# Performance work log

Measured on AMD Instinct MI355X. Metric: run time of the kernel, lower is better.

## Reference

```python
import jax, jax.numpy as jnp
import numpy as np

D_MODEL = 512
B, T = 2, 4096
LN_EPS = 1e-5


def _layernorm(x, gamma, beta):
    mu = jnp.mean(x, axis=-1, keepdims=True)
    var = jnp.mean((x - mu) ** 2, axis=-1, keepdims=True)
    return (x - mu) * jax.lax.rsqrt(var + LN_EPS) * gamma + beta


def setup_inputs() -> dict:
    key = jax.random.key(0)
    ks = jax.random.split(key, 16)
    d = D_MODEL
    s = 1.0 / np.sqrt(d)
    inp = {
        "tokens": jax.random.normal(ks[0], (B, T, d), dtype=jnp.float32),
        "Wq": jax.random.normal(ks[1], (d, d), dtype=jnp.float32) * s,
        "bq": jnp.zeros((d,), jnp.float32),
        "Wk": jax.random.normal(ks[2], (d, d), dtype=jnp.float32) * s,
        "bk": jnp.zeros((d,), jnp.float32),
        "Wv": jax.random.normal(ks[3], (d, d), dtype=jnp.float32) * s,
        "bv": jnp.zeros((d,), jnp.float32),
        "distance_scale": jnp.asarray(0.01, jnp.float32),
        "W1": jax.random.normal(ks[4], (d, 4 * d), dtype=jnp.float32) * s,
        "b1": jnp.zeros((4 * d,), jnp.float32),
        "W2": jax.random.normal(ks[5], (4 * d, d), dtype=jnp.float32) * (1.0 / np.sqrt(4 * d)),
        "b2": jnp.zeros((d,), jnp.float32),
        "g1": jnp.ones((d,), jnp.float32),
        "be1": jnp.zeros((d,), jnp.float32),
        "g2": jnp.ones((d,), jnp.float32),
        "be2": jnp.zeros((d,), jnp.float32),
    }
    return inp


def reference(tokens, Wq, bq, Wk, bk, Wv, bv, distance_scale,
              W1, b1, W2, b2, g1, be1, g2, be2):
    Bv, Tv, d = tokens.shape
    q = tokens @ Wq + bq
    k = tokens @ Wk + bk
    v = tokens @ Wv + bv
    # [B, T, T] raw scores
    scores = jnp.einsum('btd,bsd->bts', q, k)
    pos = jnp.arange(Tv)
    distance = jnp.abs(pos[None, :] - pos[:, None]).astype(jnp.float32)  # [T, T]
    scores = scores + (-distance_scale * distance)[None, :, :]
    causal = pos[None, :] > pos[:, None]  # strict upper triangle
    scores = jnp.where(causal[None, :, :], -jnp.inf, scores)
    scores = scores / jnp.sqrt(jnp.asarray(d, jnp.float32))
    attn = jax.nn.softmax(scores, axis=-1)
    attn_out = jnp.einsum('bts,bsd->btd', attn, v)
    x = _layernorm(tokens + attn_out, g1, be1)
    y = jnp.maximum(x @ W1 + b1, 0.0) @ W2 + b2
    z = _layernorm(y + x, g2, be2)
    return z
```

## Files before the change

### kernel.cpp

```cpp
#include <hip/hip_runtime.h>
#include <hip/hip_bf16.h>
#include <math.h>

typedef unsigned short u16;
typedef __attribute__((ext_vector_type(8))) short short8;
typedef __attribute__((ext_vector_type(4))) float float4v;

#define MFMA_BF16(a, b, c) __builtin_amdgcn_mfma_f32_16x16x32_bf16((a), (b), (c), 0, 0, 0)

typedef const __attribute__((address_space(1))) void* gas_ptr;
typedef __attribute__((address_space(3))) void* las_ptr;

__device__ __forceinline__ u16 f2bf(float f) {
  __hip_bfloat16 h = __float2bfloat16(f);
  return __builtin_bit_cast(u16, h);
}

__device__ __forceinline__ float bf2f(u16 v) {
  return __builtin_bit_cast(float, (unsigned)v << 16);
}

__device__ __forceinline__ void load_lds16(const u16* g, u16* l) {
  __builtin_amdgcn_global_load_lds((gas_ptr)g, (las_ptr)l, 16, 0, 0);
}

__device__ __forceinline__ int xcd_swz(int bid, int nwg) {
  return (bid & 7) * (nwg >> 3) + (bid >> 3);
}

__device__ __forceinline__ void gemm_mainloop(
    const u16* __restrict__ A, const u16* __restrict__ Bt,
    int kb, int kend, int lda, int ldb,
    int m0, int n0, u16* As, u16* Bs, float4v acc[4][4])
{
  const int tid = threadIdx.x;
  const int w = tid >> 6, lane = tid & 63;
  const int wr = w >> 1, wc = w & 1;
  const int lr = lane & 15, lk = (lane >> 4) * 8;
  for (int k0 = kb; k0 < kend; k0 += 32) {
#pragma unroll
    for (int c = 0; c < 2; ++c) {
      int idx = c * 256 + w * 64 + lane;
      int r = idx >> 2, c8 = idx & 3;
      load_lds16(A + (size_t)(m0 + r) * lda + k0 + c8 * 8, As + (size_t)(c * 256 + w * 64) * 8);
      load_lds16(Bt + (size_t)(n0 + r) * ldb + k0 + c8 * 8, Bs + (size_t)(c * 256 + w * 64) * 8);
    }
    __syncthreads();
    short8 af[4], bf[4];
#pragma unroll
    for (int mt = 0; mt < 4; ++mt)
      af[mt] = *(const short8*)&As[(wr * 64 + mt * 16 + lr) * 32 + lk];
#pragma unroll
    for (int nt = 0; nt < 4; ++nt)
      bf[nt] = *(const short8*)&Bs[(wc * 64 + nt * 16 + lr) * 32 + lk];
#pragma unroll
    for (int mt = 0; mt < 4; ++mt)
#pragma unroll
      for (int nt = 0; nt < 4; ++nt)
        acc[mt][nt] = MFMA_BF16(af[mt], bf[nt], acc[mt][nt]);
    __syncthreads();
  }
}

__global__ __launch_bounds__(256) void gemm_qkv(
    const u16* __restrict__ A, const u16* __restrict__ Bt,
    const float* __restrict__ bq, const float* __restrict__ bk, const float* __restrict__ bv,
    u16* __restrict__ qo, u16* __restrict__ ko, u16* __restrict__ vto)
{
  __shared__ u16 As[128 * 32], Bs[128 * 32];
  float4v acc[4][4];
#pragma unroll
  for (int mt = 0; mt < 4; ++mt)
#pragma unroll
    for (int nt = 0; nt < 4; ++nt) acc[mt][nt] = (float4v){0.f, 0.f, 0.f, 0.f};
  const int s = xcd_swz(blockIdx.x + 12 * blockIdx.y, 12 * 64);
  const int m0 = (s / 12) * 128, n0 = (s % 12) * 128;
  gemm_mainloop(A, Bt, 0, 512, 512, 512, m0, n0, As, Bs, acc);
  const int tid = threadIdx.x, w = tid >> 6, lane = tid & 63;
  const int wr = w >> 1, wc = w & 1, lr = lane & 15, lg = lane >> 4;
#pragma unroll
  for (int mt = 0; mt < 4; ++mt) {
#pragma unroll
    for (int nt = 0; nt < 4; ++nt) {
      int n = n0 + wc * 64 + nt * 16 + lr;
#pragma unroll
      for (int r = 0; r < 4; ++r) {
        int i = m0 + wr * 64 + mt * 16 + lg * 4 + r;
        float v = acc[mt][nt][r];
        if (n < 512) {
          qo[(size_t)i * 512 + n] = f2bf(v + bq[n]);
        } else if (n < 1024) {
          ko[(size_t)i * 512 + (n - 512)] = f2bf(v + bk[n - 512]);
        } else {
          int bb = i >> 12, t = i & 4095;
          vto[((size_t)(bb * 512 + (n - 1024))) * 4096 + t] = f2bf(v + bv[n - 1024]);
        }
      }
    }
  }
}

__global__ __launch_bounds__(256) void gemm_qk_p(
    const u16* __restrict__ q, const u16* __restrict__ k,
    const float* __restrict__ dsp,
    u16* __restrict__ P, float* __restrict__ l)
{
  __shared__ u16 As[128 * 32], Bs[128 * 32];
  float4v acc[4][4];
#pragma unroll
  for (int mt = 0; mt < 4; ++mt)
#pragma unroll
    for (int nt = 0; nt < 4; ++nt) acc[mt][nt] = (float4v){0.f, 0.f, 0.f, 0.f};
  const int b = blockIdx.y;
  const u16* qb = q + (size_t)b * 4096 * 512;
  const u16* kb = k + (size_t)b * 4096 * 512;
  u16* Pb = P + (size_t)b * 4096 * 4096;
  float* lb = l + b * 4096;
  int idx = blockIdx.x;
  int tm = (int)((sqrtf(8.0f * (float)idx + 1.0f) - 1.0f) * 0.5f);
  while ((tm + 1) * (tm + 2) / 2 <= idx) ++tm;
  while (tm * (tm + 1) / 2 > idx) --tm;
  int tn = idx - tm * (tm + 1) / 2;
  const int m0 = tm * 128, n0 = tn * 128;
  gemm_mainloop(qb, kb, 0, 512, 512, 512, m0, n0, As, Bs, acc);
  const int tid = threadIdx.x, w = tid >> 6, lane = tid & 63;
  const int wr = w >> 1, wc = w & 1, lr = lane & 15, lg = lane >> 4;
  const float invs = 0.04419417382415922f;
  const float dsi = dsp[0] * invs;
  const float L2E = 1.4426950408889634f;
  float rs[4][4];
#pragma unroll
  for (int mt = 0; mt < 4; ++mt)
#pragma unroll
    for (int r = 0; r < 4; ++r) rs[mt][r] = 0.f;
#pragma unroll
  for (int mt = 0; mt < 4; ++mt) {
#pragma unroll
    for (int nt = 0; nt < 4; ++nt) {
      int j = n0 + wc * 64 + nt * 16 + lr;
#pragma unroll
      for (int r = 0; r < 4; ++r) {
        int i = m0 + wr * 64 + mt * 16 + lg * 4 + r;
        float x = acc[mt][nt][r] * invs - dsi * fabsf((float)(i - j));
        float p = (j > i) ? 0.f : exp2f(x * L2E);
        Pb[(size_t)i * 4096 + j] = f2bf(p);
        rs[mt][r] += p;
      }
    }
  }
#pragma unroll
  for (int mt = 0; mt < 4; ++mt) {
#pragma unroll
    for (int r = 0; r < 4; ++r) {
      float v = rs[mt][r];
#pragma unroll
      for (int off = 1; off < 16; off <<= 1) v += __shfl_xor(v, off, 64);
      if (lr == 0)
        atomicAdd(&lb[m0 + wr * 64 + mt * 16 + lg * 4 + r], v);
    }
  }
}

__global__ __launch_bounds__(256) void gemm_pv(
    const u16* __restrict__ P, const u16* __restrict__ vt,
    float* __restrict__ y0, u16* __restrict__ y1,
    u16* __restrict__ y2, u16* __restrict__ y3)
{
  __shared__ u16 As[128 * 32], Bs[128 * 32];
  float4v acc[4][4];
#pragma unroll
  for (int mt = 0; mt < 4; ++mt)
#pragma unroll
    for (int nt = 0; nt < 4; ++nt) acc[mt][nt] = (float4v){0.f, 0.f, 0.f, 0.f};
  const int s = xcd_swz(blockIdx.x + 4 * (blockIdx.y + 80 * blockIdx.z), 640);
  const int b = s / 320;
  const int t2 = s % 320;
  const int xb = t2 % 4;
  int rem = t2 / 4;
  const u16* Pb = P + (size_t)b * 4096 * 4096;
  const u16* vb = vt + (size_t)b * 512 * 4096;
  int tm = 0, cpt = 1;
  while (rem >= cpt) { rem -= cpt; ++tm; cpt = (tm >> 3) + 1; }
  const int m0 = tm * 128, n0 = xb * 128;
  const int kb = rem * 1024;
  const int kfull = (tm + 1) * 128;
  const int kend = (kb + 1024 < kfull) ? (kb + 1024) : kfull;
  gemm_mainloop(Pb, vb, kb, kend, 4096, 4096, m0, n0, As, Bs, acc);
  const int tid = threadIdx.x, w = tid >> 6, lane = tid & 63;
  const int wr = w >> 1, wc = w & 1, lr = lane & 15, lg = lane >> 4;
  const size_t bofs = (size_t)b * 4096 * 512;
#pragma unroll
  for (int mt = 0; mt < 4; ++mt) {
#pragma unroll
    for (int nt = 0; nt < 4; ++nt) {
      int n = n0 + wc * 64 + nt * 16 + lr;
#pragma unroll
      for (int r = 0; r < 4; ++r) {
        int i = m0 + wr * 64 + mt * 16 + lg * 4 + r;
        size_t o = bofs + (size_t)i * 512 + n;
        float v = acc[mt][nt][r];
        if (rem == 0)      y0[o] = v;
        else if (rem == 1) y1[o] = f2bf(v);
        else if (rem == 2) y2[o] = f2bf(v);
        else               y3[o] = f2bf(v);
      }
    }
  }
}

__global__ __launch_bounds__(256) void gemm_ffn1(
    const u16* __restrict__ A, const u16* __restrict__ Bt,
    const float* __restrict__ b1, u16* __restrict__ h)
{
  __shared__ u16 As[128 * 32], Bs[128 * 32];
  float4v acc[4][4];
#pragma unroll
  for (int mt = 0; mt < 4; ++mt)
#pragma unroll
    for (int nt = 0; nt < 4; ++nt) acc[mt][nt] = (float4v){0.f, 0.f, 0.f, 0.f};
  const int s = xcd_swz(blockIdx.x + 16 * blockIdx.y, 16 * 64);
  const int m0 = (s / 16) * 128, n0 = (s % 16) * 128;
  gemm_mainloop(A, Bt, 0, 512, 512, 512, m0, n0, As, Bs, acc);
  const int tid = threadIdx.x, w = tid >> 6, lane = tid & 63;
  const int wr = w >> 1, wc = w & 1, lr = lane & 15, lg = lane >> 4;
#pragma unroll
  for (int mt = 0; mt < 4; ++mt) {
#pragma unroll
    for (int nt = 0; nt < 4; ++nt) {
      int n = n0 + wc * 64 + nt * 16 + lr;
#pragma unroll
      for (int r = 0; r < 4; ++r) {
        int i = m0 + wr * 64 + mt * 16 + lg * 4 + r;
        h[(size_t)i * 2048 + n] = f2bf(fmaxf(acc[mt][nt][r] + b1[n], 0.f));
      }
    }
  }
}

__global__ __launch_bounds__(256) void gemm_ffn2(
    const u16* __restrict__ A, const u16* __restrict__ Bt,
    float* __restrict__ f0, u16* __restrict__ f1)
{
  __shared__ u16 As[128 * 32], Bs[128 * 32];
  float4v acc[4][4];
#pragma unroll
  for (int mt = 0; mt < 4; ++mt)
#pragma unroll
    for (int nt = 0; nt < 4; ++nt) acc[mt][nt] = (float4v){0.f, 0.f, 0.f, 0.f};
  const int s = xcd_swz(blockIdx.x + 4 * (blockIdx.y + 64 * blockIdx.z), 512);
  const int zz = s / 256;
  const int t2 = s % 256;
  const int m0 = (t2 / 4) * 128, n0 = (t2 % 4) * 128;
  const int kb = zz * 1024;
  gemm_mainloop(A, Bt, kb, kb + 1024, 2048, 2048, m0, n0, As, Bs, acc);
  const int tid = threadIdx.x, w = tid >> 6, lane = tid & 63;
  const int wr = w >> 1, wc = w & 1, lr = lane & 15, lg = lane >> 4;
#pragma unroll
  for (int mt = 0; mt < 4; ++mt) {
#pragma unroll
    for (int nt = 0; nt < 4; ++nt) {
      int n = n0 + wc * 64 + nt * 16 + lr;
#pragma unroll
      for (int r = 0; r < 4; ++r) {
        int i = m0 + wr * 64 + mt * 16 + lg * 4 + r;
        if (zz == 0) f0[(size_t)i * 512 + n] = acc[mt][nt][r];
        else         f1[(size_t)i * 512 + n] = f2bf(acc[mt][nt][r]);
      }
    }
  }
}

__global__ __launch_bounds__(256) void ln1_kernel(
    const float* __restrict__ y0, const u16* __restrict__ y1,
    const u16* __restrict__ y2, const u16* __restrict__ y3,
    const float* __restrict__ lsum, const float* __restrict__ tok,
    const float* __restrict__ g, const float* __restrict__ be,
    float* __restrict__ of, u16* __restrict__ ob)
{
  const int row = blockIdx.x * 4 + (threadIdx.x >> 6);
  const int lane = threadIdx.x & 63;
  const int rloc = row & 4095;
  const size_t base = (size_t)row * 512 + lane * 8;
  const float linv = 1.0f / lsum[row];
  float v[8];
#pragma unroll
  for (int t = 0; t < 8; ++t) v[t] = y0[base + t];
  if (rloc >= 1024) {
#pragma unroll
    for (int t = 0; t < 8; ++t) v[t] += bf2f(y1[base + t]);
  }
  if (rloc >= 2048) {
#pragma unroll
    for (int t = 0; t < 8; ++t) v[t] += bf2f(y2[base + t]);
  }
  if (rloc >= 3072) {
#pragma unroll
    for (int t = 0; t < 8; ++t) v[t] += bf2f(y3[base + t]);
  }
#pragma unroll
  for (int t = 0; t < 8; ++t) v[t] = v[t] * linv + tok[base + t];
  float s = 0.f;
#pragma unroll
  for (int t = 0; t < 8; ++t) s += v[t];
#pragma unroll
  for (int off = 1; off < 64; off <<= 1) s += __shfl_xor(s, off, 64);
  const float mu = s * (1.0f / 512.0f);
  float qv = 0.f;
#pragma unroll
  for (int t = 0; t < 8; ++t) { float d = v[t] - mu; qv += d * d; }
#pragma unroll
  for (int off = 1; off < 64; off <<= 1) qv += __shfl_xor(qv, off, 64);
  const float rs = rsqrtf(qv * (1.0f / 512.0f) + 1e-5f);
  const int cb = lane * 8;
#pragma unroll
  for (int t = 0; t < 8; ++t) {
    float xv = (v[t] - mu) * rs * g[cb + t] + be[cb + t];
    of[base + t] = xv;
    ob[base + t] = f2bf(xv);
  }
}

__global__ __launch_bounds__(256) void ln2_kernel(
    const float* __restrict__ f0, const u16* __restrict__ f1,
    const float* __restrict__ b2, const float* __restrict__ bsrc,
    const float* __restrict__ g, const float* __restrict__ be,
    float* __restrict__ of)
{
  const int row = blockIdx.x * 4 + (threadIdx.x >> 6);
  const int lane = threadIdx.x & 63;
  const size_t base = (size_t)row * 512 + lane * 8;
  const int cb = lane * 8;
  float v[8];
#pragma unroll
  for (int t = 0; t < 8; ++t)
    v[t] = f0[base + t] + bf2f(f1[base + t]) + b2[cb + t] + bsrc[base + t];
  float s = 0.f;
#pragma unroll
  for (int t = 0; t < 8; ++t) s += v[t];
#pragma unroll
  for (int off = 1; off < 64; off <<= 1) s += __shfl_xor(s, off, 64);
  const float mu = s * (1.0f / 512.0f);
  float qv = 0.f;
#pragma unroll
  for (int t = 0; t < 8; ++t) { float d = v[t] - mu; qv += d * d; }
#pragma unroll
  for (int off = 1; off < 64; off <<= 1) qv += __shfl_xor(qv, off, 64);
  const float rs = rsqrtf(qv * (1.0f / 512.0f) + 1e-5f);
#pragma unroll
  for (int t = 0; t < 8; ++t) {
    float xv = (v[t] - mu) * rs * g[cb + t] + be[cb + t];
    of[base + t] = xv;
  }
}

__global__ __launch_bounds__(256) void cast_bf_kernel(
    const float* __restrict__ in, u16* __restrict__ out)
{
  const size_t i = ((size_t)blockIdx.x * 256 + threadIdx.x) * 8;
#pragma unroll
  for (int t = 0; t < 8; ++t) out[i + t] = f2bf(in[i + t]);
}

__global__ __launch_bounds__(256) void transpose_qkv_kernel(
    const float* __restrict__ Wq, const float* __restrict__ Wk,
    const float* __restrict__ Wv, u16* __restrict__ dst)
{
  __shared__ u16 tile[32][33];
  const float* src = (blockIdx.z == 0) ? Wq : (blockIdx.z == 1) ? Wk : Wv;
  u16* d = dst + (size_t)blockIdx.z * 512 * 512;
  const int tx = threadIdx.x & 31, ty = threadIdx.x >> 5;
  const int n0 = blockIdx.x * 32, k0 = blockIdx.y * 32;
#pragma unroll
  for (int i = 0; i < 32; i += 8)
    tile[ty + i][tx] = f2bf(src[(size_t)(k0 + ty + i) * 512 + n0 + tx]);
  __syncthreads();
#pragma unroll
  for (int i = 0; i < 32; i += 8)
    d[(size_t)(n0 + ty + i) * 512 + k0 + tx] = tile[tx][ty + i];
}

__global__ __launch_bounds__(256) void transpose_bf_kernel(
    const float* __restrict__ src, u16* __restrict__ dst, int K, int N)
{
  __shared__ u16 tile[32][33];
  const int tx = threadIdx.x & 31, ty = threadIdx.x >> 5;
  const int n0 = blockIdx.x * 32, k0 = blockIdx.y * 32;
#pragma unroll
  for (int i = 0; i < 32; i += 8)
    tile[ty + i][tx] = f2bf(src[(size_t)(k0 + ty + i) * N + n0 + tx]);
  __syncthreads();
#pragma unroll
  for (int i = 0; i < 32; i += 8)
    dst[(size_t)(n0 + ty + i) * K + k0 + tx] = tile[tx][ty + i];
}

extern "C" void kernel_launch(void* const* d_in, const int* in_sizes, int n_in,
                              void* d_out, int out_size, void* d_ws, size_t ws_size,
                              hipStream_t stream) {
  const float* tokens = (const float*)d_in[0];
  const float* Wq = (const float*)d_in[1];
  const float* bq = (const float*)d_in[2];
  const float* Wk = (const float*)d_in[3];
  const float* bk = (const float*)d_in[4];
  const float* Wv = (const float*)d_in[5];
  const float* bv = (const float*)d_in[6];
  const float* dscale = (const float*)d_in[7];
  const float* W1 = (const float*)d_in[8];
  const float* b1 = (const float*)d_in[9];
  const float* W2 = (const float*)d_in[10];
  const float* b2 = (const float*)d_in[11];
  const float* g1 = (const float*)d_in[12];
  const float* be1 = (const float*)d_in[13];
  const float* g2 = (const float*)d_in[14];
  const float* be2 = (const float*)d_in[15];
  float* out = (float*)d_out;

  char* ws = (char*)d_ws;
  u16*   tok_bf = (u16*)(ws + 0);
  u16*   wqkvT  = (u16*)(ws + 8388608);
  u16*   w1T    = (u16*)(ws + 9961472);
  u16*   w2T    = (u16*)(ws + 12058624);
  u16*   qbuf   = (u16*)(ws + 14155776);
  u16*   kbuf   = (u16*)(ws + 22544384);
  u16*   vtbuf  = (u16*)(ws + 30932992);
  u16*   Pbuf   = (u16*)(ws + 39321600);
  float* y0buf  = (float*)(ws + 106430464);
  u16*   y1buf  = (u16*)(ws + 123207680);
  u16*   y2buf  = (u16*)(ws + 131596288);
  u16*   y3buf  = (u16*)(ws + 139984896);
  float* xf     = (float*)(ws + 148373504);
  u16*   xbf    = (u16*)(ws + 165150720);
  u16*   hbuf   = (u16*)(ws + 173539328);
  float* f0buf  = (float*)(ws + 207093760);
  u16*   f1buf  = (u16*)(ws + 223870976);
  float* lbuf   = (float*)(ws + 232259584);

  (void)hipMemsetAsync(lbuf, 0, 2 * 4096 * sizeof(float), stream);

  cast_bf_kernel<<<2048, 256, 0, stream>>>(tokens, tok_bf);
  transpose_qkv_kernel<<<dim3(16, 16, 3), 256, 0, stream>>>(Wq, Wk, Wv, wqkvT);
  transpose_bf_kernel<<<dim3(64, 16), 256, 0, stream>>>(W1, w1T, 512, 2048);
  transpose_bf_kernel<<<dim3(16, 64), 256, 0, stream>>>(W2, w2T, 2048, 512);

  gemm_qkv<<<dim3(12, 64), 256, 0, stream>>>(tok_bf, wqkvT, bq, bk, bv, qbuf, kbuf, vtbuf);

  gemm_qk_p<<<dim3(528, 2), 256, 0, stream>>>(qbuf, kbuf, dscale, Pbuf, lbuf);
  gemm_pv<<<dim3(4, 80, 2), 256, 0, stream>>>(Pbuf, vtbuf, y0buf, y1buf, y2buf, y3buf);

  ln1_kernel<<<2048, 256, 0, stream>>>(y0buf, y1buf, y2buf, y3buf, lbuf, tokens,
                                       g1, be1, xf, xbf);

  gemm_ffn1<<<dim3(16, 64), 256, 0, stream>>>(xbf, w1T, b1, hbuf);

  gemm_ffn2<<<dim3(4, 64, 2), 256, 0, stream>>>(hbuf, w2T, f0buf, f1buf);

  ln2_kernel<<<2048, 256, 0, stream>>>(f0buf, f1buf, b2, xf, g2, be2, out);
}
```

Baseline: 305.6 us.

## Use 256x256 double-buffered GEMM tiles with 512 threads across all matmuls

Replaces the 128x128, BK=32 single-buffered mainloop with a 256x256, BK=64 tile computed by 8 waves. It double-buffers LDS through async global-to-LDS loads and raises MFMA priority with setprio. All GEMM kernels are relaunched with the new grid decompositions, and FFN2 now uses a 4-way split-K with extra partial buffers that ln2 sums. The larger tiles aim to raise arithmetic intensity and hide load latency. In exchange they use 128KB of dynamic LDS per block and 128 accumulator registers per thread, and launch far fewer blocks, which can hurt occupancy and load balance.

```diff
diff --git a/kernel.cpp b/kernel.cpp
--- a/kernel.cpp
+++ b/kernel.cpp
@@ -28,64 +28,86 @@
   return (bid & 7) * (nwg >> 3) + (bid >> 3);
 }
 
-__device__ __forceinline__ void gemm_mainloop(
+__device__ __forceinline__ void gemm_mainloop256(
     const u16* __restrict__ A, const u16* __restrict__ Bt,
     int kb, int kend, int lda, int ldb,
-    int m0, int n0, u16* As, u16* Bs, float4v acc[4][4])
+    int m0, int n0, u16* lds, float4v acc[8][4])
 {
   const int tid = threadIdx.x;
   const int w = tid >> 6, lane = tid & 63;
-  const int wr = w >> 1, wc = w & 1;
+  const int wr = w >> 2, wc = w & 3;
   const int lr = lane & 15, lk = (lane >> 4) * 8;
-  for (int k0 = kb; k0 < kend; k0 += 32) {
-#pragma unroll
-    for (int c = 0; c < 2; ++c) {
-      int idx = c * 256 + w * 64 + lane;
-      int r = idx >> 2, c8 = idx & 3;
-      load_lds16(A + (size_t)(m0 + r) * lda + k0 + c8 * 8, As + (size_t)(c * 256 + w * 64) * 8);
-      load_lds16(Bt + (size_t)(n0 + r) * ldb + k0 + c8 * 8, Bs + (size_t)(c * 256 + w * 64) * 8);
+  const int r4 = lane >> 2, c4 = (lane & 3) * 8;
+
+  auto stage = [&](int buf, int k0) {
+#pragma unroll
+    for (int c = 0; c < 4; ++c) {
+      int ri = w + c * 8;
+      int p = ri >> 4, rg = ri & 15;
+      int row = rg * 16 + r4;
+      int col = p * 32 + c4;
+      u16* dA = lds + buf * 16384 + p * 8192 + rg * 512;
+      u16* dB = lds + 32768 + buf * 16384 + p * 8192 + rg * 512;
+      load_lds16(A + (size_t)(m0 + row) * lda + k0 + col, dA);
+      load_lds16(Bt + (size_t)(n0 + row) * ldb + k0 + col, dB);
+    }
+  };
+
+  int cur = 0;
+  stage(0, kb);
+  __syncthreads();
+  for (int k0 = kb; k0 < kend; k0 += 64) {
+    if (k0 + 64 < kend) stage(cur ^ 1, k0 + 64);
+    const u16* As = lds + cur * 16384;
+    const u16* Bs = lds + 32768 + cur * 16384;
+#pragma unroll
+    for (int ks = 0; ks < 2; ++ks) {
+      short8 af[8], bfr[4];
+#pragma unroll
+      for (int mt = 0; mt < 8; ++mt)
+        af[mt] = *(const short8*)&As[ks * 8192 + (wr * 128 + mt * 16 + lr) * 32 + lk];
+#pragma unroll
+      for (int nt = 0; nt < 4; ++nt)
+        bfr[nt] = *(const short8*)&Bs[ks * 8192 + (wc * 64 + nt * 16 + lr) * 32 + lk];
+      __builtin_amdgcn_s_setprio(1);
+#pragma unroll
+      for (int mt = 0; mt < 8; ++mt)
+#pragma unroll
+        for (int nt = 0; nt < 4; ++nt)
+          acc[mt][nt] = MFMA_BF16(af[mt], bfr[nt], acc[mt][nt]);
+      __builtin_amdgcn_s_setprio(0);
     }
     __syncthreads();
-    short8 af[4], bf[4];
-#pragma unroll
-    for (int mt = 0; mt < 4; ++mt)
-      af[mt] = *(const short8*)&As[(wr * 64 + mt * 16 + lr) * 32 + lk];
-#pragma unroll
-    for (int nt = 0; nt < 4; ++nt)
-      bf[nt] = *(const short8*)&Bs[(wc * 64 + nt * 16 + lr) * 32 + lk];
-#pragma unroll
-    for (int mt = 0; mt < 4; ++mt)
-#pragma unroll
-      for (int nt = 0; nt < 4; ++nt)
-        acc[mt][nt] = MFMA_BF16(af[mt], bf[nt], acc[mt][nt]);
-    __syncthreads();
-  }
-}
-
-__global__ __launch_bounds__(256) void gemm_qkv(
+    cur ^= 1;
+  }
+}
+
+#define ACC_INIT(acc)                                              \
+  _Pragma("unroll") for (int mt = 0; mt < 8; ++mt)                 \
+  _Pragma("unroll") for (int nt = 0; nt < 4; ++nt)                 \
+      acc[mt][nt] = (float4v){0.f, 0.f, 0.f, 0.f};
+
+__global__ __launch_bounds__(512, 2) void gemm_qkv(
     const u16* __restrict__ A, const u16* __restrict__ Bt,
     const float* __restrict__ bq, const float* __restrict__ bk, const float* __restrict__ bv,
     u16* __restrict__ qo, u16* __restrict__ ko, u16* __restrict__ vto)
 {
-  __shared__ u16 As[128 * 32], Bs[128 * 32];
-  float4v acc[4][4];
-#pragma unroll
-  for (int mt = 0; mt < 4; ++mt)
-#pragma unroll
-    for (int nt = 0; nt < 4; ++nt) acc[mt][nt] = (float4v){0.f, 0.f, 0.f, 0.f};
-  const int s = xcd_swz(blockIdx.x + 12 * blockIdx.y, 12 * 64);
-  const int m0 = (s / 12) * 128, n0 = (s % 12) * 128;
-  gemm_mainloop(A, Bt, 0, 512, 512, 512, m0, n0, As, Bs, acc);
+  extern __shared__ u16 lds[];
+  float4v acc[8][4];
+  ACC_INIT(acc);
+  const int s = xcd_swz(blockIdx.x, 192);
+  const int m0 = (s / 6) * 256, n0 = (s % 6) * 256;
+  gemm_mainloop256(A, Bt, 0, 512, 512, 512, m0, n0, lds, acc);
   const int tid = threadIdx.x, w = tid >> 6, lane = tid & 63;
-  const int wr = w >> 1, wc = w & 1, lr = lane & 15, lg = lane >> 4;
-#pragma unroll
-  for (int mt = 0; mt < 4; ++mt) {
+  const int wr = w >> 2, wc = w & 3, lr = lane & 15, lg = lane >> 4;
+#pragma unroll
+  for (int mt = 0; mt < 8; ++mt) {
 #pragma unroll
     for (int nt = 0; nt < 4; ++nt) {
       int n = n0 + wc * 64 + nt * 16 + lr;
 #pragma unroll
       for (int r = 0; r < 4; ++r) {
-        int i = m0 + wr * 64 + mt * 16 + lg * 4 + r;
+        int i = m0 + wr * 128 + mt * 16 + lg * 4 + r;
         float v = acc[mt][nt][r];
         if (n < 512) {
           qo[(size_t)i * 512 + n] = f2bf(v + bq[n]);
@@ -100,17 +122,14 @@
   }
 }
 
-__global__ __launch_bounds__(256) void gemm_qk_p(
+__global__ __launch_bounds__(512, 2) void gemm_qk_p(
     const u16* __restrict__ q, const u16* __restrict__ k,
     const float* __restrict__ dsp,
     u16* __restrict__ P, float* __restrict__ l)
 {
-  __shared__ u16 As[128 * 32], Bs[128 * 32];
-  float4v acc[4][4];
-#pragma unroll
-  for (int mt = 0; mt < 4; ++mt)
-#pragma unroll
-    for (int nt = 0; nt < 4; ++nt) acc[mt][nt] = (float4v){0.f, 0.f, 0.f, 0.f};
+  extern __shared__ u16 lds[];
+  float4v acc[8][4];
+  ACC_INIT(acc);
   const int b = blockIdx.y;
   const u16* qb = q + (size_t)b * 4096 * 512;
   const u16* kb = k + (size_t)b * 4096 * 512;
@@ -121,26 +140,26 @@
   while ((tm + 1) * (tm + 2) / 2 <= idx) ++tm;
   while (tm * (tm + 1) / 2 > idx) --tm;
   int tn = idx - tm * (tm + 1) / 2;
-  const int m0 = tm * 128, n0 = tn * 128;
-  gemm_mainloop(qb, kb, 0, 512, 512, 512, m0, n0, As, Bs, acc);
+  const int m0 = tm * 256, n0 = tn * 256;
+  gemm_mainloop256(qb, kb, 0, 512, 512, 512, m0, n0, lds, acc);
   const int tid = threadIdx.x, w = tid >> 6, lane = tid & 63;
-  const int wr = w >> 1, wc = w & 1, lr = lane & 15, lg = lane >> 4;
+  const int wr = w >> 2, wc = w & 3, lr = lane & 15, lg = lane >> 4;
   const float invs = 0.04419417382415922f;
   const float dsi = dsp[0] * invs;
   const float L2E = 1.4426950408889634f;
-  float rs[4][4];
-#pragma unroll
-  for (int mt = 0; mt < 4; ++mt)
+  float rs[8][4];
+#pragma unroll
+  for (int mt = 0; mt < 8; ++mt)
 #pragma unroll
     for (int r = 0; r < 4; ++r) rs[mt][r] = 0.f;
 #pragma unroll
-  for (int mt = 0; mt < 4; ++mt) {
+  for (int mt = 0; mt < 8; ++mt) {
 #pragma unroll
     for (int nt = 0; nt < 4; ++nt) {
       int j = n0 + wc * 64 + nt * 16 + lr;
 #pragma unroll
       for (int r = 0; r < 4; ++r) {
-        int i = m0 + wr * 64 + mt * 16 + lg * 4 + r;
+        int i = m0 + wr * 128 + mt * 16 + lg * 4 + r;
         float x = acc[mt][nt][r] * invs - dsi * fabsf((float)(i - j));
         float p = (j > i) ? 0.f : exp2f(x * L2E);
         Pb[(size_t)i * 4096 + j] = f2bf(p);
@@ -149,54 +168,51 @@
     }
   }
 #pragma unroll
-  for (int mt = 0; mt < 4; ++mt) {
+  for (int mt = 0; mt < 8; ++mt) {
 #pragma unroll
     for (int r = 0; r < 4; ++r) {
       float v = rs[mt][r];
 #pragma unroll
       for (int off = 1; off < 16; off <<= 1) v += __shfl_xor(v, off, 64);
       if (lr == 0)
-        atomicAdd(&lb[m0 + wr * 64 + mt * 16 + lg * 4 + r], v);
-    }
-  }
-}
-
-__global__ __launch_bounds__(256) void gemm_pv(
+        atomicAdd(&lb[m0 + wr * 128 + mt * 16 + lg * 4 + r], v);
+    }
+  }
+}
+
+__global__ __launch_bounds__(512, 2) void gemm_pv(
     const u16* __restrict__ P, const u16* __restrict__ vt,
     float* __restrict__ y0, u16* __restrict__ y1,
     u16* __restrict__ y2, u16* __restrict__ y3)
 {
-  __shared__ u16 As[128 * 32], Bs[128 * 32];
-  float4v acc[4][4];
-#pragma unroll
-  for (int mt = 0; mt < 4; ++mt)
-#pragma unroll
-    for (int nt = 0; nt < 4; ++nt) acc[mt][nt] = (float4v){0.f, 0.f, 0.f, 0.f};
-  const int s = xcd_swz(blockIdx.x + 4 * (blockIdx.y + 80 * blockIdx.z), 640);
-  const int b = s / 320;
-  const int t2 = s % 320;
-  const int xb = t2 % 4;
-  int rem = t2 / 4;
+  extern __shared__ u16 lds[];
+  float4v acc[8][4];
+  ACC_INIT(acc);
+  const int s = xcd_swz(blockIdx.x, 160);
+  const int b = s / 80;
+  const int t2 = s % 80;
+  const int xb = t2 & 1;
+  int rem = t2 >> 1;
   const u16* Pb = P + (size_t)b * 4096 * 4096;
   const u16* vb = vt + (size_t)b * 512 * 4096;
   int tm = 0, cpt = 1;
-  while (rem >= cpt) { rem -= cpt; ++tm; cpt = (tm >> 3) + 1; }
-  const int m0 = tm * 128, n0 = xb * 128;
+  while (rem >= cpt) { rem -= cpt; ++tm; cpt = (tm >> 2) + 1; }
+  const int m0 = tm * 256, n0 = xb * 256;
   const int kb = rem * 1024;
-  const int kfull = (tm + 1) * 128;
+  const int kfull = (tm + 1) * 256;
   const int kend = (kb + 1024 < kfull) ? (kb + 1024) : kfull;
-  gemm_mainloop(Pb, vb, kb, kend, 4096, 4096, m0, n0, As, Bs, acc);
+  gemm_mainloop256(Pb, vb, kb, kend, 4096, 4096, m0, n0, lds, acc);
   const int tid = threadIdx.x, w = tid >> 6, lane = tid & 63;
-  const int wr = w >> 1, wc = w & 1, lr = lane & 15, lg = lane >> 4;
+  const int wr = w >> 2, wc = w & 3, lr = lane & 15, lg = lane >> 4;
   const size_t bofs = (size_t)b * 4096 * 512;
 #pragma unroll
-  for (int mt = 0; mt < 4; ++mt) {
+  for (int mt = 0; mt < 8; ++mt) {
 #pragma unroll
     for (int nt = 0; nt < 4; ++nt) {
       int n = n0 + wc * 64 + nt * 16 + lr;
 #pragma unroll
       for (int r = 0; r < 4; ++r) {
-        int i = m0 + wr * 64 + mt * 16 + lg * 4 + r;
+        int i = m0 + wr * 128 + mt * 16 + lg * 4 + r;
         size_t o = bofs + (size_t)i * 512 + n;
         float v = acc[mt][nt][r];
         if (rem == 0)      y0[o] = v;
@@ -208,63 +224,63 @@
   }
 }
 
-__global__ __launch_bounds__(256) void gemm_ffn1(
+__global__ __launch_bounds__(512, 2) void gemm_ffn1(
     const u16* __restrict__ A, const u16* __restrict__ Bt,
     const float* __restrict__ b1, u16* __restrict__ h)
 {
-  __shared__ u16 As[128 * 32], Bs[128 * 32];
-  float4v acc[4][4];
-#pragma unroll
-  for (int mt = 0; mt < 4; ++mt)
-#pragma unroll
-    for (int nt = 0; nt < 4; ++nt) acc[mt][nt] = (float4v){0.f, 0.f, 0.f, 0.f};
-  const int s = xcd_swz(blockIdx.x + 16 * blockIdx.y, 16 * 64);
-  const int m0 = (s / 16) * 128, n0 = (s % 16) * 128;
-  gemm_mainloop(A, Bt, 0, 512, 512, 512, m0, n0, As, Bs, acc);
+  extern __shared__ u16 lds[];
+  float4v acc[8][4];
+  ACC_INIT(acc);
+  const int s = xcd_swz(blockIdx.x, 256);
+  const int m0 = (s / 8) * 256, n0 = (s % 8) * 256;
+  gemm_mainloop256(A, Bt, 0, 512, 512, 512, m0, n0, lds, acc);
   const int tid = threadIdx.x, w = tid >> 6, lane = tid & 63;
-  const int wr = w >> 1, wc = w & 1, lr = lane & 15, lg = lane >> 4;
-#pragma unroll
-  for (int mt = 0; mt < 4; ++mt) {
+  const int wr = w >> 2, wc = w & 3, lr = lane & 15, lg = lane >> 4;
+#pragma unroll
+  for (int mt = 0; mt < 8; ++mt) {
 #pragma unroll
     for (int nt = 0; nt < 4; ++nt) {
       int n = n0 + wc * 64 + nt * 16 + lr;
 #pragma unroll
       for (int r = 0; r < 4; ++r) {
-        int i = m0 + wr * 64 + mt * 16 + lg * 4 + r;
+        int i = m0 + wr * 128 + mt * 16 + lg * 4 + r;
         h[(size_t)i * 2048 + n] = f2bf(fmaxf(acc[mt][nt][r] + b1[n], 0.f));
       }
     }
   }
 }
 
-__global__ __launch_bounds__(256) void gemm_ffn2(
+__global__ __launch_bounds__(512, 2) void gemm_ffn2(
     const u16* __restrict__ A, const u16* __restrict__ Bt,
-    float* __restrict__ f0, u16* __restrict__ f1)
-{
-  __shared__ u16 As[128 * 32], Bs[128 * 32];
-  float4v acc[4][4];
-#pragma unroll
-  for (int mt = 0; mt < 4; ++mt)
-#pragma unroll
-    for (int nt = 0; nt < 4; ++nt) acc[mt][nt] = (float4v){0.f, 0.f, 0.f, 0.f};
-  const int s = xcd_swz(blockIdx.x + 4 * (blockIdx.y + 64 * blockIdx.z), 512);
-  const int zz = s / 256;
-  const int t2 = s % 256;
-  const int m0 = (t2 / 4) * 128, n0 = (t2 % 4) * 128;
-  const int kb = zz * 1024;
-  gemm_mainloop(A, Bt, kb, kb + 1024, 2048, 2048, m0, n0, As, Bs, acc);
+    float* __restrict__ f0, u16* __restrict__ f1,
+    u16* __restrict__ f2, u16* __restrict__ f3)
+{
+  extern __shared__ u16 lds[];
+  float4v acc[8][4];
+  ACC_INIT(acc);
+  const int s = xcd_swz(blockIdx.x, 256);
+  const int m0 = (s / 8) * 256;
+  const int sub = s % 8;
+  const int n0 = (sub >> 2) * 256;
+  const int zz = sub & 3;
+  const int kb = zz * 512;
+  gemm_mainloop256(A, Bt, kb, kb + 512, 2048, 2048, m0, n0, lds, acc);
   const int tid = threadIdx.x, w = tid >> 6, lane = tid & 63;
-  const int wr = w >> 1, wc = w & 1, lr = lane & 15, lg = lane >> 4;
-#pragma unroll
-  for (int mt = 0; mt < 4; ++mt) {
+  const int wr = w >> 2, wc = w & 3, lr = lane & 15, lg = lane >> 4;
+#pragma unroll
+  for (int mt = 0; mt < 8; ++mt) {
 #pragma unroll
     for (int nt = 0; nt < 4; ++nt) {
       int n = n0 + wc * 64 + nt * 16 + lr;
 #pragma unroll
       for (int r = 0; r < 4; ++r) {
-        int i = m0 + wr * 64 + mt * 16 + lg * 4 + r;
-        if (zz == 0) f0[(size_t)i * 512 + n] = acc[mt][nt][r];
-        else         f1[(size_t)i * 512 + n] = f2bf(acc[mt][nt][r]);
+        int i = m0 + wr * 128 + mt * 16 + lg * 4 + r;
+        size_t o = (size_t)i * 512 + n;
+        float v = acc[mt][nt][r];
+        if (zz == 0)      f0[o] = v;
+        else if (zz == 1) f1[o] = f2bf(v);
+        else if (zz == 2) f2[o] = f2bf(v);
+        else              f3[o] = f2bf(v);
       }
     }
   }
@@ -322,6 +338,7 @@
 
 __global__ __launch_bounds__(256) void ln2_kernel(
     const float* __restrict__ f0, const u16* __restrict__ f1,
+    const u16* __restrict__ f2, const u16* __restrict__ f3,
     const float* __restrict__ b2, const float* __restrict__ bsrc,
     const float* __restrict__ g, const float* __restrict__ be,
     float* __restrict__ of)
@@ -333,7 +350,8 @@
   float v[8];
 #pragma unroll
   for (int t = 0; t < 8; ++t)
-    v[t] = f0[base + t] + bf2f(f1[base + t]) + b2[cb + t] + bsrc[base + t];
+    v[t] = f0[base + t] + bf2f(f1[base + t]) + bf2f(f2[base + t]) + bf2f(f3[base + t])
+         + b2[cb + t] + bsrc[base + t];
   float s = 0.f;
 #pragma unroll
   for (int t = 0; t < 8; ++t) s += v[t];
@@ -433,7 +451,9 @@
   u16*   hbuf   = (u16*)(ws + 173539328);
   float* f0buf  = (float*)(ws + 207093760);
   u16*   f1buf  = (u16*)(ws + 223870976);
-  float* lbuf   = (float*)(ws + 232259584);
+  u16*   f2buf  = (u16*)(ws + 232259584);
+  u16*   f3buf  = (u16*)(ws + 240648192);
+  float* lbuf   = (float*)(ws + 249036800);
 
   (void)hipMemsetAsync(lbuf, 0, 2 * 4096 * sizeof(float), stream);
 
@@ -442,17 +462,17 @@
   transpose_bf_kernel<<<dim3(64, 16), 256, 0, stream>>>(W1, w1T, 512, 2048);
   transpose_bf_kernel<<<dim3(16, 64), 256, 0, stream>>>(W2, w2T, 2048, 512);
 
-  gemm_qkv<<<dim3(12, 64), 256, 0, stream>>>(tok_bf, wqkvT, bq, bk, bv, qbuf, kbuf, vtbuf);
-
-  gemm_qk_p<<<dim3(528, 2), 256, 0, stream>>>(qbuf, kbuf, dscale, Pbuf, lbuf);
-  gemm_pv<<<dim3(4, 80, 2), 256, 0, stream>>>(Pbuf, vtbuf, y0buf, y1buf, y2buf, y3buf);
+  gemm_qkv<<<192, 512, 131072, stream>>>(tok_bf, wqkvT, bq, bk, bv, qbuf, kbuf, vtbuf);
+
+  gemm_qk_p<<<dim3(136, 2), 512, 131072, stream>>>(qbuf, kbuf, dscale, Pbuf, lbuf);
+  gemm_pv<<<160, 512, 131072, stream>>>(Pbuf, vtbuf, y0buf, y1buf, y2buf, y3buf);
 
   ln1_kernel<<<2048, 256, 0, stream>>>(y0buf, y1buf, y2buf, y3buf, lbuf, tokens,
                                        g1, be1, xf, xbf);
 
-  gemm_ffn1<<<dim3(16, 64), 256, 0, stream>>>(xbf, w1T, b1, hbuf);
-
-  gemm_ffn2<<<dim3(4, 64, 2), 256, 0, stream>>>(hbuf, w2T, f0buf, f1buf);
-
-  ln2_kernel<<<2048, 256, 0, stream>>>(f0buf, f1buf, b2, xf, g2, be2, out);
-}
+  gemm_ffn1<<<256, 512, 131072, stream>>>(xbf, w1T, b1, hbuf);
+
+  gemm_ffn2<<<256, 512, 131072, stream>>>(hbuf, w2T, f0buf, f1buf, f2buf, f3buf);
+
+  ln2_kernel<<<2048, 256, 0, stream>>>(f0buf, f1buf, f2buf, f3buf, b2, xf, g2, be2, out);
+}
```

After: 352.3 us. +15.3%, slower.

## Double-buffer GEMM LDS staging and move V transpose to separate kernel

Applied to the files above, without the earlier changes.

The shared GEMM mainloop now uses two LDS buffers, prefetching the tile two steps ahead with async global-to-LDS loads. Explicit vmcnt/lgkmcnt waits and barriers replace the two full __syncthreads per iteration, so global loads overlap MFMA work. Separately, the QKV GEMM now writes V row-major instead of scattering a strided transpose, and a tiled LDS transpose kernel builds V^T afterwards. This doubles LDS per block, which may lower occupancy, and adds one kernel launch plus an extra pass over V.

```diff
diff --git a/kernel.cpp b/kernel.cpp
--- a/kernel.cpp
+++ b/kernel.cpp
@@ -37,37 +37,52 @@
   const int w = tid >> 6, lane = tid & 63;
   const int wr = w >> 1, wc = w & 1;
   const int lr = lane & 15, lk = (lane >> 4) * 8;
-  for (int k0 = kb; k0 < kend; k0 += 32) {
+
+  auto stage = [&](int buf, int k0) {
 #pragma unroll
     for (int c = 0; c < 2; ++c) {
       int idx = c * 256 + w * 64 + lane;
       int r = idx >> 2, c8 = idx & 3;
-      load_lds16(A + (size_t)(m0 + r) * lda + k0 + c8 * 8, As + (size_t)(c * 256 + w * 64) * 8);
-      load_lds16(Bt + (size_t)(n0 + r) * ldb + k0 + c8 * 8, Bs + (size_t)(c * 256 + w * 64) * 8);
-    }
-    __syncthreads();
+      load_lds16(A + (size_t)(m0 + r) * lda + k0 + c8 * 8,
+                 As + buf * 4096 + (size_t)(c * 256 + w * 64) * 8);
+      load_lds16(Bt + (size_t)(n0 + r) * ldb + k0 + c8 * 8,
+                 Bs + buf * 4096 + (size_t)(c * 256 + w * 64) * 8);
+    }
+  };
+
+  const int nt = (kend - kb) >> 5;
+  stage(0, kb);
+  if (nt > 1) stage(1, kb + 32);
+  for (int t = 0; t < nt; ++t) {
+    if (t + 1 < nt) asm volatile("s_waitcnt vmcnt(4)\n\ts_barrier" ::: "memory");
+    else            asm volatile("s_waitcnt vmcnt(0)\n\ts_barrier" ::: "memory");
+    const u16* Ab = As + (t & 1) * 4096;
+    const u16* Bb = Bs + (t & 1) * 4096;
     short8 af[4], bf[4];
 #pragma unroll
     for (int mt = 0; mt < 4; ++mt)
-      af[mt] = *(const short8*)&As[(wr * 64 + mt * 16 + lr) * 32 + lk];
-#pragma unroll
-    for (int nt = 0; nt < 4; ++nt)
-      bf[nt] = *(const short8*)&Bs[(wc * 64 + nt * 16 + lr) * 32 + lk];
+      af[mt] = *(const short8*)&Ab[(wr * 64 + mt * 16 + lr) * 32 + lk];
+#pragma unroll
+    for (int nt2 = 0; nt2 < 4; ++nt2)
+      bf[nt2] = *(const short8*)&Bb[(wc * 64 + nt2 * 16 + lr) * 32 + lk];
 #pragma unroll
     for (int mt = 0; mt < 4; ++mt)
 #pragma unroll
-      for (int nt = 0; nt < 4; ++nt)
-        acc[mt][nt] = MFMA_BF16(af[mt], bf[nt], acc[mt][nt]);
-    __syncthreads();
+      for (int nt2 = 0; nt2 < 4; ++nt2)
+        acc[mt][nt2] = MFMA_BF16(af[mt], bf[nt2], acc[mt][nt2]);
+    if (t + 2 < nt) {
+      asm volatile("s_waitcnt lgkmcnt(0)\n\ts_barrier" ::: "memory");
+      stage(t & 1, kb + (t + 2) * 32);
+    }
   }
 }
 
 __global__ __launch_bounds__(256) void gemm_qkv(
     const u16* __restrict__ A, const u16* __restrict__ Bt,
     const float* __restrict__ bq, const float* __restrict__ bk, const float* __restrict__ bv,
-    u16* __restrict__ qo, u16* __restrict__ ko, u16* __restrict__ vto)
-{
-  __shared__ u16 As[128 * 32], Bs[128 * 32];
+    u16* __restrict__ qo, u16* __restrict__ ko, u16* __restrict__ vo)
+{
+  __shared__ u16 As[2 * 128 * 32], Bs[2 * 128 * 32];
   float4v acc[4][4];
 #pragma unroll
   for (int mt = 0; mt < 4; ++mt)
@@ -92,12 +107,29 @@
         } else if (n < 1024) {
           ko[(size_t)i * 512 + (n - 512)] = f2bf(v + bk[n - 512]);
         } else {
-          int bb = i >> 12, t = i & 4095;
-          vto[((size_t)(bb * 512 + (n - 1024))) * 4096 + t] = f2bf(v + bv[n - 1024]);
+          vo[(size_t)i * 512 + (n - 1024)] = f2bf(v + bv[n - 1024]);
         }
       }
     }
   }
+}
+
+__global__ __launch_bounds__(256) void transpose_v_kernel(
+    const u16* __restrict__ src, u16* __restrict__ dst)
+{
+  __shared__ u16 tile[32][33];
+  const int b = blockIdx.z;
+  const int t0 = blockIdx.x * 32, d0 = blockIdx.y * 32;
+  const u16* sp = src + (size_t)b * 4096 * 512;
+  u16* dp = dst + (size_t)b * 512 * 4096;
+  const int tx = threadIdx.x & 31, ty = threadIdx.x >> 5;
+#pragma unroll
+  for (int i = 0; i < 32; i += 8)
+    tile[ty + i][tx] = sp[(size_t)(t0 + ty + i) * 512 + d0 + tx];
+  __syncthreads();
+#pragma unroll
+  for (int i = 0; i < 32; i += 8)
+    dp[(size_t)(d0 + ty + i) * 4096 + t0 + tx] = tile[tx][ty + i];
 }
 
 __global__ __launch_bounds__(256) void gemm_qk_p(
@@ -105,7 +137,7 @@
     const float* __restrict__ dsp,
     u16* __restrict__ P, float* __restrict__ l)
 {
-  __shared__ u16 As[128 * 32], Bs[128 * 32];
+  __shared__ u16 As[2 * 128 * 32], Bs[2 * 128 * 32];
   float4v acc[4][4];
 #pragma unroll
   for (int mt = 0; mt < 4; ++mt)
@@ -166,7 +198,7 @@
     float* __restrict__ y0, u16* __restrict__ y1,
     u16* __restrict__ y2, u16* __restrict__ y3)
 {
-  __shared__ u16 As[128 * 32], Bs[128 * 32];
+  __shared__ u16 As[2 * 128 * 32], Bs[2 * 128 * 32];
   float4v acc[4][4];
 #pragma unroll
   for (int mt = 0; mt < 4; ++mt)
@@ -212,7 +244,7 @@
     const u16* __restrict__ A, const u16* __restrict__ Bt,
     const float* __restrict__ b1, u16* __restrict__ h)
 {
-  __shared__ u16 As[128 * 32], Bs[128 * 32];
+  __shared__ u16 As[2 * 128 * 32], Bs[2 * 128 * 32];
   float4v acc[4][4];
 #pragma unroll
   for (int mt = 0; mt < 4; ++mt)
@@ -241,7 +273,7 @@
     const u16* __restrict__ A, const u16* __restrict__ Bt,
     float* __restrict__ f0, u16* __restrict__ f1)
 {
-  __shared__ u16 As[128 * 32], Bs[128 * 32];
+  __shared__ u16 As[2 * 128 * 32], Bs[2 * 128 * 32];
   float4v acc[4][4];
 #pragma unroll
   for (int mt = 0; mt < 4; ++mt)
@@ -434,6 +466,7 @@
   float* f0buf  = (float*)(ws + 207093760);
   u16*   f1buf  = (u16*)(ws + 223870976);
   float* lbuf   = (float*)(ws + 232259584);
+  u16*   vbuf   = (u16*)(ws + 232292352);
 
   (void)hipMemsetAsync(lbuf, 0, 2 * 4096 * sizeof(float), stream);
 
@@ -442,7 +475,8 @@
   transpose_bf_kernel<<<dim3(64, 16), 256, 0, stream>>>(W1, w1T, 512, 2048);
   transpose_bf_kernel<<<dim3(16, 64), 256, 0, stream>>>(W2, w2T, 2048, 512);
 
-  gemm_qkv<<<dim3(12, 64), 256, 0, stream>>>(tok_bf, wqkvT, bq, bk, bv, qbuf, kbuf, vtbuf);
+  gemm_qkv<<<dim3(12, 64), 256, 0, stream>>>(tok_bf, wqkvT, bq, bk, bv, qbuf, kbuf, vbuf);
+  transpose_v_kernel<<<dim3(128, 16, 2), 256, 0, stream>>>(vbuf, vtbuf);
 
   gemm_qk_p<<<dim3(528, 2), 256, 0, stream>>>(qbuf, kbuf, dscale, Pbuf, lbuf);
   gemm_pv<<<dim3(4, 80, 2), 256, 0, stream>>>(Pbuf, vtbuf, y0buf, y1buf, y2buf, y3buf);
```

New measurement: 308.9 us. No clear change (+1.1%).
